# Kernel tuning notes

Hardware: AMD Instinct MI355X
Metric: run time of the kernel (lower is better)

The kernel has to match this reference:

```python
import jax, jax.numpy as jnp
import numpy as np
import math

D_MODEL = 1024
N_HEAD = 16
D_K = D_MODEL // N_HEAD  # 64
SEQ = 1024
BATCH = 8


def setup_inputs() -> dict:
    k = jax.random.key(0)
    ks = jax.random.split(k, 11)
    f32 = jnp.float32
    scale = 1.0 / math.sqrt(D_MODEL)
    return {
        "query": jax.random.normal(ks[0], (BATCH, SEQ, D_MODEL), dtype=f32),
        "key": jax.random.normal(ks[1], (BATCH, SEQ, D_MODEL), dtype=f32),
        "value": jax.random.normal(ks[2], (BATCH, SEQ, D_MODEL), dtype=f32),
        # Shaw-style relative position table a[q_pos, k_pos, d_k]
        "rel": jax.random.normal(ks[3], (SEQ, SEQ, D_K), dtype=f32) * 0.02,
        "W_q": jax.random.normal(ks[4], (D_MODEL, D_MODEL), dtype=f32) * scale,
        "b_q": jnp.zeros((D_MODEL,), dtype=f32),
        "W_k": jax.random.normal(ks[5], (D_MODEL, D_MODEL), dtype=f32) * scale,
        "b_k": jnp.zeros((D_MODEL,), dtype=f32),
        "W_v": jax.random.normal(ks[6], (D_MODEL, D_MODEL), dtype=f32) * scale,
        "b_v": jnp.zeros((D_MODEL,), dtype=f32),
        # boolean mask: True = masked out (matches torch masked_fill semantics)
        "mask": jax.random.randint(ks[7], (BATCH, SEQ, SEQ), 0, 4) == 0,
    }


def reference(query, key, value, rel, W_q, b_q, W_k, b_k, W_v, b_v, mask):
    B, S, D = query.shape
    H, dk = N_HEAD, D // N_HEAD

    def proj(x, W, b):
        # [B,S,D] -> [B,H,S,dk]
        return (x @ W + b).reshape(B, S, H, dk).transpose(0, 2, 1, 3)

    Q = proj(query, W_q, b_q)
    K = proj(key, W_k, b_k)
    V = proj(value, W_v, b_v)

    # E_1 = Q K^T / sqrt(d_k): [B,H,Sq,Sk]
    scores = jnp.einsum("bhqd,bhkd->bhqk", Q, K) / math.sqrt(dk)
    # E_2 = Q x relative_position (per query position), added UNscaled as in source
    scores = scores + jnp.einsum("bhqd,qkd->bhqk", Q, rel)
    # masked_fill(mask, -1e8)
    scores = jnp.where(mask[:, None, :, :], jnp.float32(-1e8), scores)
    attn = jax.nn.softmax(scores, axis=-1)
    out = jnp.einsum("bhqk,bhkd->bhqd", attn, V)  # [B,H,S,dk]
    return out.transpose(0, 2, 1, 3).reshape(B, S, D)
```

## Files before the change

### kernel.cpp

```cpp
#include <hip/hip_runtime.h>

typedef _Float16 h8_t __attribute__((ext_vector_type(8)));
typedef _Float16 h4_t __attribute__((ext_vector_type(4)));
typedef float f4_t __attribute__((ext_vector_type(4)));

#define MFMA16(a, b, c) __builtin_amdgcn_mfma_f32_16x16x32_f16((a), (b), (c), 0, 0, 0)

__device__ inline void gl_lds16(const _Float16* g, _Float16* l) {
    __builtin_amdgcn_global_load_lds(
        (const __attribute__((address_space(1))) unsigned int*)g,
        (__attribute__((address_space(3))) unsigned int*)l, 16, 0, 0);
}

__global__ void cvt4(const float* __restrict__ in, _Float16* __restrict__ out, int n4) {
    int i = blockIdx.x * 256 + threadIdx.x;
    if (i < n4) {
        f4_t v = *(const f4_t*)(in + (size_t)i * 4);
        h4_t h;
        for (int j = 0; j < 4; ++j) h[j] = (_Float16)v[j];
        *(h4_t*)(out + (size_t)i * 4) = h;
    }
}

__global__ void wtrans(const float* __restrict__ W, _Float16* __restrict__ Wt) {
    __shared__ float tile[32][33];
    int tid = threadIdx.x;
    int tx = tid & 31, ty = tid >> 5;
    int nb = blockIdx.x * 32, kb = blockIdx.y * 32;
    for (int p = 0; p < 4; ++p)
        tile[ty + p * 8][tx] = W[(size_t)(kb + ty + p * 8) * 1024 + nb + tx];
    __syncthreads();
    for (int p = 0; p < 4; ++p)
        Wt[(size_t)(nb + ty + p * 8) * 1024 + kb + tx] = (_Float16)tile[tx][ty + p * 8];
}

__global__ __launch_bounds__(256, 2) void proj_gemm(
    const _Float16* __restrict__ X, const _Float16* __restrict__ Wt,
    const float* __restrict__ bias, _Float16* __restrict__ Out,
    float scale, int vmode)
{
    __shared__ __align__(16) _Float16 Asm[128 * 32];
    __shared__ __align__(16) _Float16 Bsm[128 * 32];
    int tid = threadIdx.x;
    int wave = tid >> 6, lane = tid & 63;
    int l15 = lane & 15, quad = lane >> 4;
    int m0 = blockIdx.x * 128, n0 = blockIdx.y * 128;
    int wm = (wave >> 1) * 64, wn = (wave & 1) * 64;
    f4_t acc[4][4] = {};
    int f0 = wave * 128 + lane;

    for (int kt = 0; kt < 1024; kt += 32) {
        for (int j = 0; j < 2; ++j) {
            int f = f0 + j * 64;
            int r = f >> 2, c = (f & 3) * 8;
            gl_lds16(&X[(size_t)(m0 + r) * 1024 + kt + c], &Asm[f * 8]);
            gl_lds16(&Wt[(size_t)(n0 + r) * 1024 + kt + c], &Bsm[f * 8]);
        }
        __syncthreads();
        h8_t af[4], bf[4];
        for (int i = 0; i < 4; ++i) af[i] = *(const h8_t*)&Asm[(wm + i * 16 + l15) * 32 + quad * 8];
        for (int j = 0; j < 4; ++j) bf[j] = *(const h8_t*)&Bsm[(wn + j * 16 + l15) * 32 + quad * 8];
        for (int i = 0; i < 4; ++i)
            for (int j = 0; j < 4; ++j)
                acc[i][j] = MFMA16(af[i], bf[j], acc[i][j]);
        __syncthreads();
    }
    for (int j = 0; j < 4; ++j) {
        int n = n0 + wn + j * 16 + l15;
        float bv = bias[n];
        int h = n >> 6, d = n & 63;
        for (int i = 0; i < 4; ++i) {
            for (int r = 0; r < 4; ++r) {
                int m = m0 + wm + i * 16 + quad * 4 + r;
                int bb = m >> 10, ss = m & 1023;
                float v = (acc[i][j][r] + bv) * scale;
                size_t oidx = vmode ? (((size_t)(bb * 16 + h) * 64 + d) * 1024 + ss)
                                    : (((size_t)(bb * 16 + h) * 1024 + ss) * 64 + d);
                Out[oidx] = (_Float16)v;
            }
        }
    }
}

__device__ inline h8_t ld_rel(const _Float16* relh, const float* relf, size_t idx) {
    if (relh) return *(const h8_t*)(relh + idx);
    f4_t a = *(const f4_t*)(relf + idx);
    f4_t b = *(const f4_t*)(relf + idx + 4);
    h8_t h;
    for (int j = 0; j < 4; ++j) { h[j] = (_Float16)a[j]; h[4 + j] = (_Float16)b[j]; }
    return h;
}

__global__ __launch_bounds__(256, 2) void attn_kernel(
    const _Float16* __restrict__ Qh,
    const _Float16* __restrict__ Kh,
    const _Float16* __restrict__ Vt,
    const _Float16* __restrict__ relh,
    const float* __restrict__ relf,
    const int* __restrict__ mask,
    float* __restrict__ out)
{
    __shared__ __align__(16) _Float16 R_lds[2][16][17][36];
    __shared__ __align__(16) _Float16 P_lds[16][16][40];

    const int tid = threadIdx.x;
    const int wave = tid >> 6, lane = tid & 63;
    const int l15 = lane & 15, quad = lane >> 4;
    const int b = blockIdx.y;
    const int q0 = blockIdx.x * 16;

    h8_t bQ[4][2];
    h8_t bR[4][2];
    for (int gi = 0; gi < 4; ++gi) {
        int g = wave * 4 + gi;
        const _Float16* qp = Qh + ((size_t)(b * 16 + g) * 1024 + q0 + l15) * 64 + quad * 8;
        bQ[gi][0] = *(const h8_t*)qp;
        bQ[gi][1] = *(const h8_t*)(qp + 32);
    }
    for (int qi = 0; qi < 4; ++qi) {
        int q = q0 + wave * 4 + qi;
        const _Float16* qp = Qh + ((size_t)(b * 16 + l15) * 1024 + q) * 64 + quad * 8;
        bR[qi][0] = *(const h8_t*)qp;
        bR[qi][1] = *(const h8_t*)(qp + 32);
    }

    f4_t acc[4][4] = {};
    float mst[4], lst[4];
    for (int gi = 0; gi < 4; ++gi) { mst[gi] = -1e30f; lst[gi] = 0.0f; }

    int buf = 0;
    for (int t0 = 0; t0 < 1024; t0 += 32, buf ^= 1) {
        const int* mrow = &mask[((size_t)b * 1024 + q0 + l15) * 1024 + t0];
        int4 mk0 = *(const int4*)(mrow + quad * 4);
        int4 mk1 = *(const int4*)(mrow + 16 + quad * 4);

        h8_t relv[4][2][2];
        for (int qi = 0; qi < 4; ++qi) {
            size_t rb = ((size_t)(q0 + wave * 4 + qi) * 1024 + t0 + l15) * 64 + quad * 8;
            relv[qi][0][0] = ld_rel(relh, relf, rb);
            relv[qi][0][1] = ld_rel(relh, relf, rb + 32);
            relv[qi][1][0] = ld_rel(relh, relf, rb + 1024);
            relv[qi][1][1] = ld_rel(relh, relf, rb + 1056);
        }
        for (int qi = 0; qi < 4; ++qi) {
            for (int tm = 0; tm < 2; ++tm) {
                f4_t c = {0.f, 0.f, 0.f, 0.f};
                c = MFMA16(relv[qi][tm][0], bR[qi][0], c);
                c = MFMA16(relv[qi][tm][1], bR[qi][1], c);
                h4_t h;
                for (int r = 0; r < 4; ++r) h[r] = (_Float16)c[r];
                *(h4_t*)&R_lds[buf][wave * 4 + qi][l15][tm * 16 + quad * 4] = h;
            }
        }

        h8_t kv[4][2][2];
        for (int gi = 0; gi < 4; ++gi) {
            const _Float16* kp =
                Kh + ((size_t)(b * 16 + wave * 4 + gi) * 1024 + t0 + l15) * 64 + quad * 8;
            kv[gi][0][0] = *(const h8_t*)kp;
            kv[gi][0][1] = *(const h8_t*)(kp + 32);
            kv[gi][1][0] = *(const h8_t*)(kp + 1024);
            kv[gi][1][1] = *(const h8_t*)(kp + 1056);
        }
        __syncthreads();

        int mm[8] = {mk0.x, mk0.y, mk0.z, mk0.w, mk1.x, mk1.y, mk1.z, mk1.w};

        for (int gi = 0; gi < 4; ++gi) {
            int g = wave * 4 + gi;
            f4_t s[2];
            for (int tm = 0; tm < 2; ++tm) {
                h4_t rh = *(const h4_t*)&R_lds[buf][l15][g][tm * 16 + quad * 4];
                f4_t c;
                for (int r = 0; r < 4; ++r) c[r] = (float)rh[r];
                c = MFMA16(kv[gi][tm][0], bQ[gi][0], c);
                c = MFMA16(kv[gi][tm][1], bQ[gi][1], c);
                s[tm] = c;
            }
            for (int tm = 0; tm < 2; ++tm)
                for (int r = 0; r < 4; ++r)
                    if (mm[tm * 4 + r]) s[tm][r] = -1e8f;

            float mx = s[0][0];
            for (int tm = 0; tm < 2; ++tm)
                for (int r = 0; r < 4; ++r) mx = fmaxf(mx, s[tm][r]);
            mx = fmaxf(mx, __shfl_xor(mx, 16));
            mx = fmaxf(mx, __shfl_xor(mx, 32));
            float mnew = fmaxf(mst[gi], mx);
            float alpha = __expf(mst[gi] - mnew);
            mst[gi] = mnew;
            float rs = 0.0f;
            for (int tm = 0; tm < 2; ++tm)
                for (int r = 0; r < 4; ++r) {
                    float p = __expf(s[tm][r] - mnew);
                    s[tm][r] = p;
                    rs += p;
                }
            rs += __shfl_xor(rs, 16);
            rs += __shfl_xor(rs, 32);
            lst[gi] = lst[gi] * alpha + rs;
            for (int dm = 0; dm < 4; ++dm) acc[gi][dm] *= alpha;
            for (int tm = 0; tm < 2; ++tm) {
                h4_t h;
                for (int r = 0; r < 4; ++r) h[r] = (_Float16)s[tm][r];
                *(h4_t*)&P_lds[g][l15][tm * 16 + quad * 4] = h;
            }
        }

        h8_t vv[4][4];
        for (int gi = 0; gi < 4; ++gi) {
            const _Float16* vp =
                Vt + (size_t)(b * 16 + wave * 4 + gi) * 65536 + t0 + quad * 8;
            for (int dm = 0; dm < 4; ++dm)
                vv[gi][dm] = *(const h8_t*)(vp + (size_t)(dm * 16 + l15) * 1024);
        }
        for (int gi = 0; gi < 4; ++gi) {
            h8_t bp = *(const h8_t*)&P_lds[wave * 4 + gi][l15][quad * 8];
            for (int dm = 0; dm < 4; ++dm)
                acc[gi][dm] = MFMA16(vv[gi][dm], bp, acc[gi][dm]);
        }
    }

    for (int gi = 0; gi < 4; ++gi) {
        int g = wave * 4 + gi;
        float linv = 1.0f / lst[gi];
        for (int dm = 0; dm < 4; ++dm) {
            f4_t v = acc[gi][dm] * linv;
            float* op = out + ((size_t)b * 1024 + q0 + l15) * 1024 + g * 64 + dm * 16 + quad * 4;
            *(f4_t*)op = v;
        }
    }
}

extern "C" void kernel_launch(void* const* d_in, const int* in_sizes, int n_in,
                              void* d_out, int out_size, void* d_ws, size_t ws_size,
                              hipStream_t stream) {
    const float* q    = (const float*)d_in[0];
    const float* k    = (const float*)d_in[1];
    const float* v    = (const float*)d_in[2];
    const float* rel  = (const float*)d_in[3];
    const float* Wq   = (const float*)d_in[4];
    const float* bq   = (const float*)d_in[5];
    const float* Wk   = (const float*)d_in[6];
    const float* bk   = (const float*)d_in[7];
    const float* Wv   = (const float*)d_in[8];
    const float* bv   = (const float*)d_in[9];
    const int*   mask = (const int*)d_in[10];
    float* out = (float*)d_out;

    const size_t NEL = 8ull * 1024 * 1024;
    const size_t WEL = 1024ull * 1024;
    const size_t RELE = 1024ull * 1024 * 64;

    char* w = (char*)d_ws;
    size_t off = 0;
    auto alloc = [&](size_t bytes) { char* p = w + off; off += bytes; return p; };
    _Float16* qx  = (_Float16*)alloc(NEL * 2);
    _Float16* kx  = (_Float16*)alloc(NEL * 2);
    _Float16* vx  = (_Float16*)alloc(NEL * 2);
    _Float16* Wqt = (_Float16*)alloc(WEL * 2);
    _Float16* Wkt = (_Float16*)alloc(WEL * 2);
    _Float16* Wvt = (_Float16*)alloc(WEL * 2);
    _Float16* Qh  = (_Float16*)alloc(NEL * 2);
    _Float16* Kh  = (_Float16*)alloc(NEL * 2);
    _Float16* Vth = (_Float16*)alloc(NEL * 2);
    _Float16* relh = nullptr;
    if (ws_size >= off + RELE * 2) relh = (_Float16*)alloc(RELE * 2);

    cvt4<<<(int)(NEL / 4 / 256), 256, 0, stream>>>(q, qx, (int)(NEL / 4));
    cvt4<<<(int)(NEL / 4 / 256), 256, 0, stream>>>(k, kx, (int)(NEL / 4));
    cvt4<<<(int)(NEL / 4 / 256), 256, 0, stream>>>(v, vx, (int)(NEL / 4));
    if (relh)
        cvt4<<<(int)(RELE / 4 / 256), 256, 0, stream>>>(rel, relh, (int)(RELE / 4));

    dim3 tg(32, 32);
    wtrans<<<tg, 256, 0, stream>>>(Wq, Wqt);
    wtrans<<<tg, 256, 0, stream>>>(Wk, Wkt);
    wtrans<<<tg, 256, 0, stream>>>(Wv, Wvt);

    dim3 pg(64, 8);
    proj_gemm<<<pg, 256, 0, stream>>>(qx, Wqt, bq, Qh, 1.0f, 0);
    proj_gemm<<<pg, 256, 0, stream>>>(kx, Wkt, bk, Kh, 0.125f, 0);
    proj_gemm<<<pg, 256, 0, stream>>>(vx, Wvt, bv, Vth, 1.0f, 1);

    dim3 ag(64, 8);
    attn_kernel<<<ag, 256, 0, stream>>>(Qh, Kh, Vth, relh, rel, mask, out);
}
```

Before: 943.2 us.

## Pack mask to bits, stage projection stores via LDS, hoist V loads, remap grid

```diff
diff --git a/kernel.cpp b/kernel.cpp
--- a/kernel.cpp
+++ b/kernel.cpp
@@ -20,6 +20,12 @@
         for (int j = 0; j < 4; ++j) h[j] = (_Float16)v[j];
         *(h4_t*)(out + (size_t)i * 4) = h;
     }
+}
+
+__global__ void packmask(const int* __restrict__ m, unsigned long long* __restrict__ out) {
+    int gid = blockIdx.x * 256 + threadIdx.x;
+    unsigned long long bal = __ballot(m[gid] != 0);
+    if ((threadIdx.x & 63) == 0) out[gid >> 6] = bal;
 }
 
 __global__ void wtrans(const float* __restrict__ W, _Float16* __restrict__ Wt) {
@@ -65,19 +71,46 @@
                 acc[i][j] = MFMA16(af[i], bf[j], acc[i][j]);
         __syncthreads();
     }
-    for (int j = 0; j < 4; ++j) {
-        int n = n0 + wn + j * 16 + l15;
-        float bv = bias[n];
-        int h = n >> 6, d = n & 63;
+
+    float bvv[4];
+    for (int j = 0; j < 4; ++j) bvv[j] = bias[n0 + wn + j * 16 + l15];
+    int hcol = (n0 + wn) >> 6;
+    _Float16* sc = (wave < 2 ? Asm : Bsm) + (wave & 1) * 2048;
+    int row = lane >> 3, co = (lane & 7) * 8;
+
+    if (vmode == 0) {
         for (int i = 0; i < 4; ++i) {
-            for (int r = 0; r < 4; ++r) {
-                int m = m0 + wm + i * 16 + quad * 4 + r;
+            for (int j = 0; j < 4; ++j)
+                for (int r = 0; r < 4; ++r)
+                    sc[(quad * 4 + r) * 72 + j * 16 + l15] =
+                        (_Float16)((acc[i][j][r] + bvv[j]) * scale);
+            __syncthreads();
+            for (int p = 0; p < 2; ++p) {
+                int rr = row + p * 8;
+                h8_t vv = *(const h8_t*)&sc[rr * 72 + co];
+                int m = m0 + wm + i * 16 + rr;
                 int bb = m >> 10, ss = m & 1023;
-                float v = (acc[i][j][r] + bv) * scale;
-                size_t oidx = vmode ? (((size_t)(bb * 16 + h) * 64 + d) * 1024 + ss)
-                                    : (((size_t)(bb * 16 + h) * 1024 + ss) * 64 + d);
-                Out[oidx] = (_Float16)v;
-            }
+                *(h8_t*)&Out[(((size_t)(bb * 16 + hcol)) * 1024 + ss) * 64 + co] = vv;
+            }
+            __syncthreads();
+        }
+    } else {
+        int mb2 = m0 + wm;
+        int bb = mb2 >> 10, ss0 = mb2 & 1023;
+        for (int j = 0; j < 4; ++j) {
+            for (int i = 0; i < 4; ++i) {
+                h4_t h;
+                for (int r = 0; r < 4; ++r) h[r] = (_Float16)((acc[i][j][r] + bvv[j]) * scale);
+                *(h4_t*)&sc[l15 * 72 + i * 16 + quad * 4] = h;
+            }
+            __syncthreads();
+            for (int p = 0; p < 2; ++p) {
+                int rr = row + p * 8;
+                h8_t vv = *(const h8_t*)&sc[rr * 72 + co];
+                int d = j * 16 + rr;
+                *(h8_t*)&Out[(((size_t)(bb * 16 + hcol)) * 64 + d) * 1024 + ss0 + co] = vv;
+            }
+            __syncthreads();
         }
     }
 }
@@ -91,13 +124,14 @@
     return h;
 }
 
-__global__ __launch_bounds__(256, 2) void attn_kernel(
+__global__ __launch_bounds__(256, 2) __attribute__((amdgpu_waves_per_eu(2, 2)))
+void attn_kernel(
     const _Float16* __restrict__ Qh,
     const _Float16* __restrict__ Kh,
     const _Float16* __restrict__ Vt,
     const _Float16* __restrict__ relh,
     const float* __restrict__ relf,
-    const int* __restrict__ mask,
+    const unsigned* __restrict__ mbits,
     float* __restrict__ out)
 {
     __shared__ __align__(16) _Float16 R_lds[2][16][17][36];
@@ -106,8 +140,8 @@
     const int tid = threadIdx.x;
     const int wave = tid >> 6, lane = tid & 63;
     const int l15 = lane & 15, quad = lane >> 4;
-    const int b = blockIdx.y;
-    const int q0 = blockIdx.x * 16;
+    const int b = blockIdx.x & 7;
+    const int q0 = (blockIdx.x >> 3) * 16;
 
     h8_t bQ[4][2];
     h8_t bR[4][2];
@@ -130,9 +164,7 @@
 
     int buf = 0;
     for (int t0 = 0; t0 < 1024; t0 += 32, buf ^= 1) {
-        const int* mrow = &mask[((size_t)b * 1024 + q0 + l15) * 1024 + t0];
-        int4 mk0 = *(const int4*)(mrow + quad * 4);
-        int4 mk1 = *(const int4*)(mrow + 16 + quad * 4);
+        unsigned mb = mbits[(((size_t)b * 1024 + q0 + l15) * 1024 + t0) >> 5];
 
         h8_t relv[4][2][2];
         for (int qi = 0; qi < 4; ++qi) {
@@ -162,9 +194,14 @@
             kv[gi][1][0] = *(const h8_t*)(kp + 1024);
             kv[gi][1][1] = *(const h8_t*)(kp + 1056);
         }
+        h8_t vv[4][4];
+        for (int gi = 0; gi < 4; ++gi) {
+            const _Float16* vp =
+                Vt + (size_t)(b * 16 + wave * 4 + gi) * 65536 + t0 + quad * 8;
+            for (int dm = 0; dm < 4; ++dm)
+                vv[gi][dm] = *(const h8_t*)(vp + (size_t)(dm * 16 + l15) * 1024);
+        }
         __syncthreads();
-
-        int mm[8] = {mk0.x, mk0.y, mk0.z, mk0.w, mk1.x, mk1.y, mk1.z, mk1.w};
 
         for (int gi = 0; gi < 4; ++gi) {
             int g = wave * 4 + gi;
@@ -179,7 +216,7 @@
             }
             for (int tm = 0; tm < 2; ++tm)
                 for (int r = 0; r < 4; ++r)
-                    if (mm[tm * 4 + r]) s[tm][r] = -1e8f;
+                    if ((mb >> (tm * 16 + quad * 4 + r)) & 1) s[tm][r] = -1e8f;
 
             float mx = s[0][0];
             for (int tm = 0; tm < 2; ++tm)
@@ -207,13 +244,6 @@
             }
         }
 
-        h8_t vv[4][4];
-        for (int gi = 0; gi < 4; ++gi) {
-            const _Float16* vp =
-                Vt + (size_t)(b * 16 + wave * 4 + gi) * 65536 + t0 + quad * 8;
-            for (int dm = 0; dm < 4; ++dm)
-                vv[gi][dm] = *(const h8_t*)(vp + (size_t)(dm * 16 + l15) * 1024);
-        }
         for (int gi = 0; gi < 4; ++gi) {
             h8_t bp = *(const h8_t*)&P_lds[wave * 4 + gi][l15][quad * 8];
             for (int dm = 0; dm < 4; ++dm)
@@ -251,6 +281,7 @@
     const size_t NEL = 8ull * 1024 * 1024;
     const size_t WEL = 1024ull * 1024;
     const size_t RELE = 1024ull * 1024 * 64;
+    const size_t MEL = 8ull * 1024 * 1024;
 
     char* w = (char*)d_ws;
     size_t off = 0;
@@ -264,6 +295,7 @@
     _Float16* Qh  = (_Float16*)alloc(NEL * 2);
     _Float16* Kh  = (_Float16*)alloc(NEL * 2);
     _Float16* Vth = (_Float16*)alloc(NEL * 2);
+    unsigned* mbits = (unsigned*)alloc(MEL / 8);
     _Float16* relh = nullptr;
     if (ws_size >= off + RELE * 2) relh = (_Float16*)alloc(RELE * 2);
 
@@ -273,6 +305,8 @@
     if (relh)
         cvt4<<<(int)(RELE / 4 / 256), 256, 0, stream>>>(rel, relh, (int)(RELE / 4));
 
+    packmask<<<(int)(MEL / 256), 256, 0, stream>>>(mask, (unsigned long long*)mbits);
+
     dim3 tg(32, 32);
     wtrans<<<tg, 256, 0, stream>>>(Wq, Wqt);
     wtrans<<<tg, 256, 0, stream>>>(Wk, Wkt);
@@ -283,6 +317,5 @@
     proj_gemm<<<pg, 256, 0, stream>>>(kx, Wkt, bk, Kh, 0.125f, 0);
     proj_gemm<<<pg, 256, 0, stream>>>(vx, Wvt, bv, Vth, 1.0f, 1);
 
-    dim3 ag(64, 8);
-    attn_kernel<<<ag, 256, 0, stream>>>(Qh, Kh, Vth, relh, rel, mask, out);
-}
+    attn_kernel<<<512, 256, 0, stream>>>(Qh, Kh, Vth, relh, rel, mbits, out);
+}
```

Measured after the change: 1.087 ms. +15.3%, slower.
